# Kernel optimization log

Measured on AMD Instinct MI355X. Metric: run time of the kernel, lower is better.

The kernel has to match this reference:

```python
import jax, jax.numpy as jnp
import numpy as np

N_HEADS = 16
HEAD_DIM = 64
ROPE_THETA = 10000.0


def rotate_half(x):
    x1, x2 = jnp.split(x, 2, axis=-1)
    return jnp.concatenate([-x2, x1], axis=-1)


def setup_inputs() -> dict:
    key = jax.random.key(0)
    k0, k1, k2 = jax.random.split(key, 3)
    B, L, C = 2, 2048, 1024
    x = jax.random.normal(k0, (B, L, C), dtype=jnp.float32)
    # causal additive bias, as used by VAR-style blockwise masks (here full causal)
    causal = jnp.tril(jnp.ones((L, L), dtype=bool))
    attn_bias = jnp.where(causal, 0.0, -1e9).astype(jnp.float32)[None, None]
    position_ids = jnp.broadcast_to(jnp.arange(L, dtype=jnp.int32), (B, L))
    qkv_w = 0.02 * jax.random.normal(k1, (3 * C, C), dtype=jnp.float32)
    q_bias = jnp.zeros((C,), jnp.float32)
    v_bias = jnp.zeros((C,), jnp.float32)
    proj_w = 0.02 * jax.random.normal(k2, (C, C), dtype=jnp.float32)
    proj_b = jnp.zeros((C,), jnp.float32)
    return {"x": x, "attn_bias": attn_bias, "position_ids": position_ids,
            "qkv_w": qkv_w, "q_bias": q_bias, "v_bias": v_bias,
            "proj_w": proj_w, "proj_b": proj_b}


def reference(x, attn_bias, position_ids, qkv_w, q_bias, v_bias, proj_w, proj_b):
    B, L, C = x.shape
    H, D = N_HEADS, HEAD_DIM
    # fused QKV projection with concatenated (q_bias, 0, v_bias)
    bias = jnp.concatenate([q_bias, jnp.zeros_like(q_bias), v_bias])
    qkv = (jnp.einsum('blc,oc->blo', x, qkv_w) + bias).reshape(B, L, 3, H, D)
    q = jnp.transpose(qkv[:, :, 0], (0, 2, 1, 3))  # [B,H,L,D]
    k = jnp.transpose(qkv[:, :, 1], (0, 2, 1, 3))
    v = jnp.transpose(qkv[:, :, 2], (0, 2, 1, 3))
    # Llama rotary embedding: cos/sin [B,L,D] -> unsqueeze dim=1
    inv_freq = 1.0 / (ROPE_THETA ** (jnp.arange(0, D, 2, dtype=jnp.float32) / D))
    freqs = position_ids.astype(jnp.float32)[:, :, None] * inv_freq  # [B,L,D/2]
    emb = jnp.concatenate([freqs, freqs], axis=-1)
    cos = jnp.cos(emb)[:, None]  # [B,1,L,D]
    sin = jnp.sin(emb)[:, None]
    q = q * cos + rotate_half(q) * sin
    k = k * cos + rotate_half(k) * sin
    # slow_attn: (q*scale) @ k^T + bias -> softmax -> @ v
    scale = 0.25 / np.sqrt(D).astype(np.float32)
    attn = jnp.einsum('bhqd,bhkd->bhqk', q * scale, k) + attn_bias
    attn = jax.nn.softmax(attn, axis=-1)
    out = jnp.einsum('bhqk,bhkd->bhqd', attn, v)
    out = out.transpose(0, 2, 1, 3).reshape(B, L, C)
    return jnp.einsum('blc,oc->blo', out, proj_w) + proj_b
```

## Files before the change

### kernel.cpp

```cpp
#include <hip/hip_runtime.h>

typedef unsigned short u16;
typedef unsigned int u32;
typedef __attribute__((ext_vector_type(8))) short short8;
typedef __attribute__((ext_vector_type(4))) float f32x4;
typedef __attribute__((ext_vector_type(2))) unsigned int u32x2;
typedef __attribute__((ext_vector_type(4))) unsigned short u16x4;
typedef __attribute__((ext_vector_type(8))) unsigned short u16x8;

#define AS1 __attribute__((address_space(1)))
#define AS3 __attribute__((address_space(3)))

__device__ __forceinline__ u16 f2bf(float f) {
  u32 u = __builtin_bit_cast(u32, f);
  u32 r = u + 0x7FFFu + ((u >> 16) & 1u);
  return (u16)(r >> 16);
}
__device__ __forceinline__ float bf2f(u16 h) {
  u32 u = ((u32)h) << 16;
  return __builtin_bit_cast(float, u);
}
__device__ __forceinline__ void gload_lds16(const void* g, void* l) {
  __builtin_amdgcn_global_load_lds((AS1 void*)g, (AS3 void*)l, 16, 0, 0);
}

__device__ __forceinline__ void cvt_body(const float* __restrict__ src, u16* __restrict__ dst,
                                         int i) {
  float4 v = ((const float4*)src)[i];
  u16x4 o;
  o[0] = f2bf(v.x); o[1] = f2bf(v.y); o[2] = f2bf(v.z); o[3] = f2bf(v.w);
  ((u16x4*)dst)[i] = o;
}

__global__ __launch_bounds__(256)
void pre_kernel(const float* __restrict__ x, const float* __restrict__ w1,
                const float* __restrict__ w2, const int* __restrict__ pos,
                u16* __restrict__ x_bf, u16* __restrict__ w1_bf, u16* __restrict__ w2_bf,
                float* __restrict__ tab) {
  int bid = blockIdx.x;
  int t = threadIdx.x;
  if (bid < 4096) {
    cvt_body(x, x_bf, bid * 256 + t);
  } else if (bid < 7168) {
    cvt_body(w1, w1_bf, (bid - 4096) * 256 + t);
  } else if (bid < 8192) {
    cvt_body(w2, w2_bf, (bid - 7168) * 256 + t);
  } else {
    int idx = (bid - 8192) * 256 + t;
    int i = idx & 31;
    int bl = idx >> 5;
    float p = (float)pos[bl];
    float inv_freq = 1.0f / powf(10000.0f, (2.0f * (float)i) / 64.0f);
    float ang = p * inv_freq;
    tab[(size_t)bl * 64 + i] = cosf(ang);
    tab[(size_t)bl * 64 + 32 + i] = sinf(ang);
  }
}

template <bool OUT_BF16>
__global__ __launch_bounds__(256)
void gemm_bt_kernel(const u16* __restrict__ A, const u16* __restrict__ Bw,
                    void* __restrict__ Cout, const float* __restrict__ bias,
                    int M, int N, int K, int NXT) {
  __shared__ alignas(16) u16 As[128 * 64];
  __shared__ alignas(16) u16 Bs[128 * 64];
  const int tid = threadIdx.x;
  const int lane = tid & 63, wave = tid >> 6;
  const int wr = wave >> 1, wc = wave & 1;
  const int nblk = gridDim.x;
  const int lin = (blockIdx.x & 7) * (nblk >> 3) + (blockIdx.x >> 3);
  const int m0 = (lin / NXT) * 128, n0 = (lin % NXT) * 128;
  const int r = lane & 15, g = lane >> 4;

  f32x4 acc[4][4] = {};

  const int nk = K >> 6;
  for (int kt = 0; kt < nk; ++kt) {
    const int k0 = kt << 6;
#pragma unroll
    for (int c = 0; c < 4; ++c) {
      int i = c * 256 + tid;
      int row = i >> 3, slot = i & 7;
      int ss = slot ^ (row & 7);
      const u16* gA = A + (size_t)(m0 + row) * K + k0 + ss * 8;
      const u16* gB = Bw + (size_t)(n0 + row) * K + k0 + ss * 8;
      void* lA = (char*)As + c * 4096 + wave * 1024;
      void* lB = (char*)Bs + c * 4096 + wave * 1024;
      gload_lds16(gA, lA);
      gload_lds16(gB, lB);
    }
    __syncthreads();
#pragma unroll
    for (int kk = 0; kk < 2; ++kk) {
      short8 af[4], bf[4];
#pragma unroll
      for (int m = 0; m < 4; ++m) {
        int row = wr * 64 + m * 16 + r;
        int byte = row * 128 + (((kk * 4 + g) ^ (row & 7)) << 4);
        af[m] = *(const short8*)((const char*)As + byte);
      }
#pragma unroll
      for (int n = 0; n < 4; ++n) {
        int row = wc * 64 + n * 16 + r;
        int byte = row * 128 + (((kk * 4 + g) ^ (row & 7)) << 4);
        bf[n] = *(const short8*)((const char*)Bs + byte);
      }
#pragma unroll
      for (int m = 0; m < 4; ++m)
#pragma unroll
        for (int n = 0; n < 4; ++n)
          acc[m][n] = __builtin_amdgcn_mfma_f32_16x16x32_bf16(af[m], bf[n], acc[m][n], 0, 0, 0);
    }
    __syncthreads();
  }

  if constexpr (OUT_BF16) {
    u16* C = (u16*)Cout;
#pragma unroll
    for (int m = 0; m < 4; ++m) {
      int rg = m0 + wr * 64 + m * 16 + g * 4;
#pragma unroll
      for (int n = 0; n < 4; ++n) {
        int cg = n0 + wc * 64 + n * 16 + r;
#pragma unroll
        for (int j = 0; j < 4; ++j)
          C[(size_t)(rg + j) * N + cg] = f2bf(acc[m][n][j]);
      }
    }
  } else {
    float* C = (float*)Cout;
#pragma unroll
    for (int m = 0; m < 4; ++m) {
      int rg = m0 + wr * 64 + m * 16 + g * 4;
#pragma unroll
      for (int n = 0; n < 4; ++n) {
        int cg = n0 + wc * 64 + n * 16 + r;
        float bv = bias[cg];
#pragma unroll
        for (int j = 0; j < 4; ++j)
          C[(size_t)(rg + j) * N + cg] = acc[m][n][j] + bv;
      }
    }
  }
}

__global__ __launch_bounds__(256)
void gemm_bt64_kernel(const u16* __restrict__ A, const u16* __restrict__ Bw,
                      float* __restrict__ Cout, const float* __restrict__ bias,
                      int M, int N, int K, int NXT) {
  __shared__ alignas(16) u16 As[128 * 64];
  __shared__ alignas(16) u16 Bs[64 * 64];
  const int tid = threadIdx.x;
  const int lane = tid & 63, wave = tid >> 6;
  const int wr = wave >> 1, wc = wave & 1;
  const int nblk = gridDim.x;
  const int lin = (blockIdx.x & 7) * (nblk >> 3) + (blockIdx.x >> 3);
  const int m0 = (lin / NXT) * 128, n0 = (lin % NXT) * 64;
  const int r = lane & 15, g = lane >> 4;

  f32x4 acc[4][2] = {};

  const int nk = K >> 6;
  for (int kt = 0; kt < nk; ++kt) {
    const int k0 = kt << 6;
#pragma unroll
    for (int c = 0; c < 4; ++c) {
      int i = c * 256 + tid;
      int row = i >> 3, slot = i & 7;
      int ss = slot ^ (row & 7);
      const u16* gA = A + (size_t)(m0 + row) * K + k0 + ss * 8;
      void* lA = (char*)As + c * 4096 + wave * 1024;
      gload_lds16(gA, lA);
    }
#pragma unroll
    for (int c = 0; c < 2; ++c) {
      int i = c * 256 + tid;
      int row = i >> 3, slot = i & 7;
      int ss = slot ^ (row & 7);
      const u16* gB = Bw + (size_t)(n0 + row) * K + k0 + ss * 8;
      void* lB = (char*)Bs + c * 4096 + wave * 1024;
      gload_lds16(gB, lB);
    }
    __syncthreads();
#pragma unroll
    for (int kk = 0; kk < 2; ++kk) {
      short8 af[4], bf[2];
#pragma unroll
      for (int m = 0; m < 4; ++m) {
        int row = wr * 64 + m * 16 + r;
        int byte = row * 128 + (((kk * 4 + g) ^ (row & 7)) << 4);
        af[m] = *(const short8*)((const char*)As + byte);
      }
#pragma unroll
      for (int n = 0; n < 2; ++n) {
        int row = wc * 32 + n * 16 + r;
        int byte = row * 128 + (((kk * 4 + g) ^ (row & 7)) << 4);
        bf[n] = *(const short8*)((const char*)Bs + byte);
      }
#pragma unroll
      for (int m = 0; m < 4; ++m)
#pragma unroll
        for (int n = 0; n < 2; ++n)
          acc[m][n] = __builtin_amdgcn_mfma_f32_16x16x32_bf16(af[m], bf[n], acc[m][n], 0, 0, 0);
    }
    __syncthreads();
  }

#pragma unroll
  for (int m = 0; m < 4; ++m) {
    int rg = m0 + wr * 64 + m * 16 + g * 4;
#pragma unroll
    for (int n = 0; n < 2; ++n) {
      int cg = n0 + wc * 32 + n * 16 + r;
      float bv = bias[cg];
#pragma unroll
      for (int j = 0; j < 4; ++j)
        Cout[(size_t)(rg + j) * N + cg] = acc[m][n][j] + bv;
    }
  }
}

#define QSCALE 0.04508422002778011f
__global__ __launch_bounds__(256)
void mid_kernel(const u16* __restrict__ qkv, const float* __restrict__ tab,
                const float* __restrict__ q_bias, const float* __restrict__ v_bias,
                u16* __restrict__ Qo, u16* __restrict__ Ko, u16* __restrict__ vt) {
  __shared__ alignas(16) u16 tile[64][72];
  int bid = blockIdx.x;
  int t = threadIdx.x;
  if (bid < 4096) {
    int bl = bid;
    int b = bl >> 11, l = bl & 2047;
    const float* tr = tab + (size_t)bl * 64;
    const u16* base = qkv + (size_t)bl * 3072;
#pragma unroll
    for (int pp = 0; pp < 2; ++pp) {
      int p = t + pp * 256;
      int h = p >> 5, d = p & 31;
      float c = tr[d], s = tr[32 + d];
      size_t o = ((size_t)(b * 16 + h) * 2048 + l) * 64 + d;
      float x1 = bf2f(base[h * 64 + d]) + q_bias[h * 64 + d];
      float x2 = bf2f(base[h * 64 + d + 32]) + q_bias[h * 64 + d + 32];
      Qo[o]      = f2bf((x1 * c - x2 * s) * QSCALE);
      Qo[o + 32] = f2bf((x2 * c + x1 * s) * QSCALE);
      x1 = bf2f(base[1024 + h * 64 + d]);
      x2 = bf2f(base[1024 + h * 64 + d + 32]);
      Ko[o]      = f2bf(x1 * c - x2 * s);
      Ko[o + 32] = f2bf(x2 * c + x1 * s);
    }
  } else {
    int bid2 = bid - 4096;
    int bh = bid2 >> 5;
    int b = bh >> 4, h = bh & 15;
    int l0 = (bid2 & 31) * 64;
    int rr = t >> 2;
    int c0 = (t & 3) * 16;
    const u16* src = qkv + ((size_t)(b * 2048 + l0 + rr)) * 3072 + 2048 + h * 64 + c0;
    u16x8 a = *(const u16x8*)src;
    u16x8 bb = *(const u16x8*)(src + 8);
#pragma unroll
    for (int i = 0; i < 8; ++i) {
      a[i]  = f2bf(bf2f(a[i])  + v_bias[h * 64 + c0 + i]);
      bb[i] = f2bf(bf2f(bb[i]) + v_bias[h * 64 + c0 + 8 + i]);
    }
    *(u16x8*)&tile[rr][c0] = a;
    *(u16x8*)&tile[rr][c0 + 8] = bb;
    __syncthreads();
    int d = t >> 2;
    int lc = (t & 3) * 16;
    u16x8 o1, o2;
#pragma unroll
    for (int i = 0; i < 8; ++i) {
      o1[i] = tile[lc + i][d];
      o2[i] = tile[lc + 8 + i][d];
    }
    u16* dst = vt + ((size_t)bh * 64 + d) * 2048 + l0 + lc;
    *(u16x8*)dst = o1;
    *(u16x8*)(dst + 8) = o2;
  }
}

__global__ __launch_bounds__(256)
void attn_kernel(const u16* __restrict__ Q, const u16* __restrict__ Kmat,
                 const u16* __restrict__ Vt, u16* __restrict__ O) {
  __shared__ alignas(16) u16 Ks[2][64 * 64];
  __shared__ alignas(16) u16 Vs[2][64 * 64];
  __shared__ alignas(16) u16 Pbuf[4][1024];
  const int tid = threadIdx.x;
  const int lane = tid & 63;
  const int wave = tid >> 6;
  const int id = blockIdx.x;
  const int bh = (id & 7) + 8 * ((id >> 3) >> 4);
  const int px = (id >> 3) & 15;
  const int b = bh >> 4, h = bh & 15;
  const int r = lane & 15, g = lane >> 4;

  const u16* Kb = Kmat + (size_t)bh * 2048 * 64;
  const u16* Vb = Vt + (size_t)bh * 64 * 2048;

  const int srow0 = tid >> 3;
  const int sslot0 = (tid & 7) ^ (srow0 & 7);
  const int srow1 = srow0 + 32;
  const int sslot1 = (tid & 7) ^ (srow1 & 7);

  u16* Pw = Pbuf[wave];

  for (int seg = 0; seg < 2; ++seg) {
    const int xq = seg ? (31 - px) : px;
    const int qrow0 = xq * 64 + wave * 16;
    const int nt = xq + 1;
    const u16* Qb = Q + ((size_t)bh * 2048 + qrow0) * 64;

    short8 qf[2];
#pragma unroll
    for (int kk = 0; kk < 2; ++kk)
      qf[kk] = *(const short8*)(Qb + r * 64 + kk * 32 + g * 8);

    f32x4 o_acc[4] = {};
    float l_run = 0.f;

    gload_lds16(Kb + (size_t)srow0 * 64 + sslot0 * 8, (char*)Ks[0] + wave * 1024);
    gload_lds16(Kb + (size_t)srow1 * 64 + sslot1 * 8, (char*)Ks[0] + 4096 + wave * 1024);
    gload_lds16(Vb + (size_t)srow0 * 2048 + sslot0 * 8, (char*)Vs[0] + wave * 1024);
    gload_lds16(Vb + (size_t)srow1 * 2048 + sslot1 * 8, (char*)Vs[0] + 4096 + wave * 1024);
    __syncthreads();

    int cur = 0;
    for (int t = 0; t < nt; ++t) {
      const int kv0 = t * 64;
      if (t + 1 < nt) {
        const u16* gK = Kb + (size_t)(kv0 + 64) * 64;
        const u16* gV = Vb + (kv0 + 64);
        char* lK = (char*)Ks[cur ^ 1];
        char* lV = (char*)Vs[cur ^ 1];
        gload_lds16(gK + (size_t)srow0 * 64 + sslot0 * 8, lK + wave * 1024);
        gload_lds16(gK + (size_t)srow1 * 64 + sslot1 * 8, lK + 4096 + wave * 1024);
        gload_lds16(gV + (size_t)srow0 * 2048 + sslot0 * 8, lV + wave * 1024);
        gload_lds16(gV + (size_t)srow1 * 2048 + sslot1 * 8, lV + 4096 + wave * 1024);
      }

      f32x4 s[4] = {};
      __builtin_amdgcn_s_setprio(1);
#pragma unroll
      for (int ct = 0; ct < 4; ++ct) {
#pragma unroll
        for (int kk = 0; kk < 2; ++kk) {
          int row = ct * 16 + r;
          int byte = row * 128 + (((kk * 4 + g) ^ (row & 7)) << 4);
          short8 kf = *(const short8*)((const char*)Ks[cur] + byte);
          s[ct] = __builtin_amdgcn_mfma_f32_16x16x32_bf16(kf, qf[kk], s[ct], 0, 0, 0);
        }
      }
      __builtin_amdgcn_s_setprio(0);

      if (kv0 + 63 > qrow0) {
        int qrow = qrow0 + r;
#pragma unroll
        for (int ct = 0; ct < 4; ++ct)
#pragma unroll
          for (int j = 0; j < 4; ++j) {
            int kv = kv0 + ct * 16 + 4 * g + j;
            if (kv > qrow) s[ct][j] = -1e30f;
          }
      }

      u32x2 pk[4];
#pragma unroll
      for (int ct = 0; ct < 4; ++ct) {
        float p0 = exp2f(s[ct][0]);
        float p1 = exp2f(s[ct][1]);
        float p2 = exp2f(s[ct][2]);
        float p3 = exp2f(s[ct][3]);
        l_run += (p0 + p1) + (p2 + p3);
        u32 lo, hi;
        asm("v_cvt_pk_bf16_f32 %0, %1, %2" : "=v"(lo) : "v"(p0), "v"(p1));
        asm("v_cvt_pk_bf16_f32 %0, %1, %2" : "=v"(hi) : "v"(p2), "v"(p3));
        pk[ct][0] = lo;
        pk[ct][1] = hi;
      }

#pragma unroll
      for (int ct = 0; ct < 4; ++ct) {
        int byte = r * 128 + ((32 * ct + 8 * g) ^ ((r & 7) << 4));
        *(u32x2*)((char*)Pw + byte) = pk[ct];
      }

      __builtin_amdgcn_s_setprio(1);
#pragma unroll
      for (int kk = 0; kk < 2; ++kk) {
        int byte = r * 128 + (((kk * 4 + g) ^ (r & 7)) << 4);
        short8 pf = *(const short8*)((const char*)Pw + byte);
#pragma unroll
        for (int n = 0; n < 4; ++n) {
          int row = n * 16 + r;
          int vbyte = row * 128 + (((kk * 4 + g) ^ (row & 7)) << 4);
          short8 vf = *(const short8*)((const char*)Vs[cur] + vbyte);
          o_acc[n] = __builtin_amdgcn_mfma_f32_16x16x32_bf16(pf, vf, o_acc[n], 0, 0, 0);
        }
      }
      __builtin_amdgcn_s_setprio(0);

      __syncthreads();
      cur ^= 1;
    }

    l_run += __shfl_xor(l_run, 16, 64);
    l_run += __shfl_xor(l_run, 32, 64);
    float linv = 1.0f / l_run;
    float ij[4];
#pragma unroll
    for (int j = 0; j < 4; ++j) ij[j] = __shfl(linv, 4 * g + j, 64);
#pragma unroll
    for (int n = 0; n < 4; ++n)
#pragma unroll
      for (int j = 0; j < 4; ++j) {
        size_t idx = ((size_t)b * 2048 + qrow0 + 4 * g + j) * 1024 + h * 64 + n * 16 + r;
        O[idx] = f2bf(o_acc[n][j] * ij[j]);
      }
  }
}

extern "C" void kernel_launch(void* const* d_in, const int* in_sizes, int n_in,
                              void* d_out, int out_size, void* d_ws, size_t ws_size,
                              hipStream_t stream) {
  const float* x      = (const float*)d_in[0];
  const int*   pos    = (const int*)d_in[2];
  const float* qkv_w  = (const float*)d_in[3];
  const float* q_bias = (const float*)d_in[4];
  const float* v_bias = (const float*)d_in[5];
  const float* proj_w = (const float*)d_in[6];
  const float* proj_b = (const float*)d_in[7];
  float* out = (float*)d_out;

  char* ws = (char*)d_ws;
  u16* x_bf    = (u16*)(ws + 0);
  u16* w1_bf   = (u16*)(ws + 8388608);
  u16* w2_bf   = (u16*)(ws + 14680064);
  u16* qkv_bf  = (u16*)(ws + 16777216);
  u16* q_bf    = (u16*)(ws + 41943040);
  u16* k_bf    = (u16*)(ws + 50331648);
  u16* vt_bf   = (u16*)(ws + 58720256);
  u16* attn_bf = (u16*)(ws + 67108864);
  float* tab   = (float*)(ws + 75497472);

  pre_kernel<<<8704, 256, 0, stream>>>(x, qkv_w, proj_w, pos, x_bf, w1_bf, w2_bf, tab);
  gemm_bt_kernel<true><<<768, 256, 0, stream>>>(x_bf, w1_bf, qkv_bf, nullptr,
                                                4096, 3072, 1024, 24);
  mid_kernel<<<5120, 256, 0, stream>>>(qkv_bf, tab, q_bias, v_bias, q_bf, k_bf, vt_bf);
  attn_kernel<<<512, 256, 0, stream>>>(q_bf, k_bf, vt_bf, attn_bf);
  gemm_bt64_kernel<<<512, 256, 0, stream>>>(attn_bf, w2_bf, out, proj_b,
                                            4096, 1024, 1024, 16);
}
```

Before: 122.3 us.

## Fuse bias and RoPE into QKV GEMM epilogue and split attention blocks

The QKV GEMM epilogue now applies q/v biases, rotary embedding and the Q scale, and writes Q and K directly in head-major layout. V is written compactly and transposed by a slimmer kernel, which removes the round trip through the full bf16 qkv buffer in the old mid kernel. The RoPE table is stored as interleaved cos/sin pairs. The attention kernel no longer processes a paired short+long query tile per block; it launches one tile per block (1024 blocks), ordered longest first, for better parallelism at the cost of less even per-block work. The epilogue now does scattered 2-byte stores and per-row table loads, which may cost some GEMM efficiency.

After: 132.0 us. +8.0%, slower.

```diff
diff --git a/kernel.cpp b/kernel.cpp
--- a/kernel.cpp
+++ b/kernel.cpp
@@ -24,6 +24,8 @@
   __builtin_amdgcn_global_load_lds((AS1 void*)g, (AS3 void*)l, 16, 0, 0);
 }
 
+#define QSCALE 0.04508422002778011f
+
 __device__ __forceinline__ void cvt_body(const float* __restrict__ src, u16* __restrict__ dst,
                                          int i) {
   float4 v = ((const float4*)src)[i];
@@ -36,7 +38,7 @@
 void pre_kernel(const float* __restrict__ x, const float* __restrict__ w1,
                 const float* __restrict__ w2, const int* __restrict__ pos,
                 u16* __restrict__ x_bf, u16* __restrict__ w1_bf, u16* __restrict__ w2_bf,
-                float* __restrict__ tab) {
+                float2* __restrict__ tab2) {
   int bid = blockIdx.x;
   int t = threadIdx.x;
   if (bid < 4096) {
@@ -52,16 +54,16 @@
     float p = (float)pos[bl];
     float inv_freq = 1.0f / powf(10000.0f, (2.0f * (float)i) / 64.0f);
     float ang = p * inv_freq;
-    tab[(size_t)bl * 64 + i] = cosf(ang);
-    tab[(size_t)bl * 64 + 32 + i] = sinf(ang);
-  }
-}
-
-template <bool OUT_BF16>
+    tab2[(size_t)bl * 32 + i] = make_float2(cosf(ang), sinf(ang));
+  }
+}
+
 __global__ __launch_bounds__(256)
-void gemm_bt_kernel(const u16* __restrict__ A, const u16* __restrict__ Bw,
-                    void* __restrict__ Cout, const float* __restrict__ bias,
-                    int M, int N, int K, int NXT) {
+void gemmqkv_kernel(const u16* __restrict__ A, const u16* __restrict__ Bw,
+                    const float* __restrict__ q_bias, const float* __restrict__ v_bias,
+                    const float2* __restrict__ tab2,
+                    u16* __restrict__ Qo, u16* __restrict__ Ko, u16* __restrict__ v_comp) {
+  const int K = 1024, NXT = 24;
   __shared__ alignas(16) u16 As[128 * 64];
   __shared__ alignas(16) u16 Bs[128 * 64];
   const int tid = threadIdx.x;
@@ -74,8 +76,7 @@
 
   f32x4 acc[4][4] = {};
 
-  const int nk = K >> 6;
-  for (int kt = 0; kt < nk; ++kt) {
+  for (int kt = 0; kt < 16; ++kt) {
     const int k0 = kt << 6;
 #pragma unroll
     for (int c = 0; c < 4; ++c) {
@@ -114,31 +115,51 @@
     __syncthreads();
   }
 
-  if constexpr (OUT_BF16) {
-    u16* C = (u16*)Cout;
+  const int cgbase = n0 + wc * 64;
+  const int seg = cgbase >> 10;
+  const int h = (cgbase & 1023) >> 6;
+
+  if (seg == 2) {
 #pragma unroll
     for (int m = 0; m < 4; ++m) {
       int rg = m0 + wr * 64 + m * 16 + g * 4;
 #pragma unroll
       for (int n = 0; n < 4; ++n) {
-        int cg = n0 + wc * 64 + n * 16 + r;
+        int c10 = (cgbase & 1023) + n * 16 + r;
+        float bv = v_bias[c10];
 #pragma unroll
         for (int j = 0; j < 4; ++j)
-          C[(size_t)(rg + j) * N + cg] = f2bf(acc[m][n][j]);
+          v_comp[(size_t)(rg + j) * 1024 + c10] = f2bf(acc[m][n][j] + bv);
       }
     }
   } else {
-    float* C = (float*)Cout;
-#pragma unroll
-    for (int m = 0; m < 4; ++m) {
-      int rg = m0 + wr * 64 + m * 16 + g * 4;
-#pragma unroll
-      for (int n = 0; n < 4; ++n) {
-        int cg = n0 + wc * 64 + n * 16 + r;
-        float bv = bias[cg];
-#pragma unroll
-        for (int j = 0; j < 4; ++j)
-          C[(size_t)(rg + j) * N + cg] = acc[m][n][j] + bv;
+    u16* Out = (seg == 0) ? Qo : Ko;
+#pragma unroll
+    for (int n2 = 0; n2 < 2; ++n2) {
+      int dlo = n2 * 16 + r;
+      float b1 = (seg == 0) ? q_bias[h * 64 + dlo] : 0.f;
+      float b2 = (seg == 0) ? q_bias[h * 64 + dlo + 32] : 0.f;
+#pragma unroll
+      for (int m = 0; m < 4; ++m) {
+        int rowbase = m0 + wr * 64 + m * 16 + g * 4;
+#pragma unroll
+        for (int j = 0; j < 4; ++j) {
+          int row = rowbase + j;
+          int bb = row >> 11, l = row & 2047;
+          float2 cs = tab2[(size_t)row * 32 + dlo];
+          float x1 = acc[m][n2][j] + b1;
+          float x2 = acc[m][n2 + 2][j] + b2;
+          float y1 = x1 * cs.x - x2 * cs.y;
+          float y2 = x2 * cs.x + x1 * cs.y;
+          size_t o = ((size_t)(bb * 16 + h) * 2048 + l) * 64 + dlo;
+          if (seg == 0) {
+            Out[o]      = f2bf(y1 * QSCALE);
+            Out[o + 32] = f2bf(y2 * QSCALE);
+          } else {
+            Out[o]      = f2bf(y1);
+            Out[o + 32] = f2bf(y2);
+          }
+        }
       }
     }
   }
@@ -220,64 +241,33 @@
   }
 }
 
-#define QSCALE 0.04508422002778011f
 __global__ __launch_bounds__(256)
-void mid_kernel(const u16* __restrict__ qkv, const float* __restrict__ tab,
-                const float* __restrict__ q_bias, const float* __restrict__ v_bias,
-                u16* __restrict__ Qo, u16* __restrict__ Ko, u16* __restrict__ vt) {
+void vtr_kernel(const u16* __restrict__ v_comp, u16* __restrict__ vt) {
   __shared__ alignas(16) u16 tile[64][72];
   int bid = blockIdx.x;
+  int bh = bid >> 5;
+  int b = bh >> 4, h = bh & 15;
+  int l0 = (bid & 31) * 64;
   int t = threadIdx.x;
-  if (bid < 4096) {
-    int bl = bid;
-    int b = bl >> 11, l = bl & 2047;
-    const float* tr = tab + (size_t)bl * 64;
-    const u16* base = qkv + (size_t)bl * 3072;
-#pragma unroll
-    for (int pp = 0; pp < 2; ++pp) {
-      int p = t + pp * 256;
-      int h = p >> 5, d = p & 31;
-      float c = tr[d], s = tr[32 + d];
-      size_t o = ((size_t)(b * 16 + h) * 2048 + l) * 64 + d;
-      float x1 = bf2f(base[h * 64 + d]) + q_bias[h * 64 + d];
-      float x2 = bf2f(base[h * 64 + d + 32]) + q_bias[h * 64 + d + 32];
-      Qo[o]      = f2bf((x1 * c - x2 * s) * QSCALE);
-      Qo[o + 32] = f2bf((x2 * c + x1 * s) * QSCALE);
-      x1 = bf2f(base[1024 + h * 64 + d]);
-      x2 = bf2f(base[1024 + h * 64 + d + 32]);
-      Ko[o]      = f2bf(x1 * c - x2 * s);
-      Ko[o + 32] = f2bf(x2 * c + x1 * s);
-    }
-  } else {
-    int bid2 = bid - 4096;
-    int bh = bid2 >> 5;
-    int b = bh >> 4, h = bh & 15;
-    int l0 = (bid2 & 31) * 64;
-    int rr = t >> 2;
-    int c0 = (t & 3) * 16;
-    const u16* src = qkv + ((size_t)(b * 2048 + l0 + rr)) * 3072 + 2048 + h * 64 + c0;
-    u16x8 a = *(const u16x8*)src;
-    u16x8 bb = *(const u16x8*)(src + 8);
-#pragma unroll
-    for (int i = 0; i < 8; ++i) {
-      a[i]  = f2bf(bf2f(a[i])  + v_bias[h * 64 + c0 + i]);
-      bb[i] = f2bf(bf2f(bb[i]) + v_bias[h * 64 + c0 + 8 + i]);
-    }
-    *(u16x8*)&tile[rr][c0] = a;
-    *(u16x8*)&tile[rr][c0 + 8] = bb;
-    __syncthreads();
-    int d = t >> 2;
-    int lc = (t & 3) * 16;
-    u16x8 o1, o2;
-#pragma unroll
-    for (int i = 0; i < 8; ++i) {
-      o1[i] = tile[lc + i][d];
-      o2[i] = tile[lc + 8 + i][d];
-    }
-    u16* dst = vt + ((size_t)bh * 64 + d) * 2048 + l0 + lc;
-    *(u16x8*)dst = o1;
-    *(u16x8*)(dst + 8) = o2;
-  }
+  int rr = t >> 2;
+  int c0 = (t & 3) * 16;
+  const u16* src = v_comp + ((size_t)(b * 2048 + l0 + rr)) * 1024 + h * 64 + c0;
+  u16x8 a = *(const u16x8*)src;
+  u16x8 bb = *(const u16x8*)(src + 8);
+  *(u16x8*)&tile[rr][c0] = a;
+  *(u16x8*)&tile[rr][c0 + 8] = bb;
+  __syncthreads();
+  int d = t >> 2;
+  int lc = (t & 3) * 16;
+  u16x8 o1, o2;
+#pragma unroll
+  for (int i = 0; i < 8; ++i) {
+    o1[i] = tile[lc + i][d];
+    o2[i] = tile[lc + 8 + i][d];
+  }
+  u16* dst = vt + ((size_t)bh * 64 + d) * 2048 + l0 + lc;
+  *(u16x8*)dst = o1;
+  *(u16x8*)(dst + 8) = o2;
 }
 
 __global__ __launch_bounds__(256)
@@ -290,8 +280,9 @@
   const int lane = tid & 63;
   const int wave = tid >> 6;
   const int id = blockIdx.x;
-  const int bh = (id & 7) + 8 * ((id >> 3) >> 4);
-  const int px = (id >> 3) & 15;
+  const int xcd = id & 7, rank = id >> 3;
+  const int bh = xcd + 8 * (rank & 3);
+  const int xq = 31 - (rank >> 2);
   const int b = bh >> 4, h = bh & 15;
   const int r = lane & 15, g = lane >> 4;
 
@@ -304,120 +295,116 @@
   const int sslot1 = (tid & 7) ^ (srow1 & 7);
 
   u16* Pw = Pbuf[wave];
-
-  for (int seg = 0; seg < 2; ++seg) {
-    const int xq = seg ? (31 - px) : px;
-    const int qrow0 = xq * 64 + wave * 16;
-    const int nt = xq + 1;
-    const u16* Qb = Q + ((size_t)bh * 2048 + qrow0) * 64;
-
-    short8 qf[2];
-#pragma unroll
-    for (int kk = 0; kk < 2; ++kk)
-      qf[kk] = *(const short8*)(Qb + r * 64 + kk * 32 + g * 8);
-
-    f32x4 o_acc[4] = {};
-    float l_run = 0.f;
-
-    gload_lds16(Kb + (size_t)srow0 * 64 + sslot0 * 8, (char*)Ks[0] + wave * 1024);
-    gload_lds16(Kb + (size_t)srow1 * 64 + sslot1 * 8, (char*)Ks[0] + 4096 + wave * 1024);
-    gload_lds16(Vb + (size_t)srow0 * 2048 + sslot0 * 8, (char*)Vs[0] + wave * 1024);
-    gload_lds16(Vb + (size_t)srow1 * 2048 + sslot1 * 8, (char*)Vs[0] + 4096 + wave * 1024);
+  const int qrow0 = xq * 64 + wave * 16;
+  const int nt = xq + 1;
+  const u16* Qb = Q + ((size_t)bh * 2048 + qrow0) * 64;
+
+  short8 qf[2];
+#pragma unroll
+  for (int kk = 0; kk < 2; ++kk)
+    qf[kk] = *(const short8*)(Qb + r * 64 + kk * 32 + g * 8);
+
+  f32x4 o_acc[4] = {};
+  float l_run = 0.f;
+
+  gload_lds16(Kb + (size_t)srow0 * 64 + sslot0 * 8, (char*)Ks[0] + wave * 1024);
+  gload_lds16(Kb + (size_t)srow1 * 64 + sslot1 * 8, (char*)Ks[0] + 4096 + wave * 1024);
+  gload_lds16(Vb + (size_t)srow0 * 2048 + sslot0 * 8, (char*)Vs[0] + wave * 1024);
+  gload_lds16(Vb + (size_t)srow1 * 2048 + sslot1 * 8, (char*)Vs[0] + 4096 + wave * 1024);
+  __syncthreads();
+
+  int cur = 0;
+  for (int t = 0; t < nt; ++t) {
+    const int kv0 = t * 64;
+    if (t + 1 < nt) {
+      const u16* gK = Kb + (size_t)(kv0 + 64) * 64;
+      const u16* gV = Vb + (kv0 + 64);
+      char* lK = (char*)Ks[cur ^ 1];
+      char* lV = (char*)Vs[cur ^ 1];
+      gload_lds16(gK + (size_t)srow0 * 64 + sslot0 * 8, lK + wave * 1024);
+      gload_lds16(gK + (size_t)srow1 * 64 + sslot1 * 8, lK + 4096 + wave * 1024);
+      gload_lds16(gV + (size_t)srow0 * 2048 + sslot0 * 8, lV + wave * 1024);
+      gload_lds16(gV + (size_t)srow1 * 2048 + sslot1 * 8, lV + 4096 + wave * 1024);
+    }
+
+    f32x4 s[4] = {};
+    __builtin_amdgcn_s_setprio(1);
+#pragma unroll
+    for (int ct = 0; ct < 4; ++ct) {
+#pragma unroll
+      for (int kk = 0; kk < 2; ++kk) {
+        int row = ct * 16 + r;
+        int byte = row * 128 + (((kk * 4 + g) ^ (row & 7)) << 4);
+        short8 kf = *(const short8*)((const char*)Ks[cur] + byte);
+        s[ct] = __builtin_amdgcn_mfma_f32_16x16x32_bf16(kf, qf[kk], s[ct], 0, 0, 0);
+      }
+    }
+    __builtin_amdgcn_s_setprio(0);
+
+    if (kv0 + 63 > qrow0) {
+      int qrow = qrow0 + r;
+#pragma unroll
+      for (int ct = 0; ct < 4; ++ct)
+#pragma unroll
+        for (int j = 0; j < 4; ++j) {
+          int kv = kv0 + ct * 16 + 4 * g + j;
+          if (kv > qrow) s[ct][j] = -1e30f;
+        }
+    }
+
+    u32x2 pk[4];
+#pragma unroll
+    for (int ct = 0; ct < 4; ++ct) {
+      float p0 = exp2f(s[ct][0]);
+      float p1 = exp2f(s[ct][1]);
+      float p2 = exp2f(s[ct][2]);
+      float p3 = exp2f(s[ct][3]);
+      l_run += (p0 + p1) + (p2 + p3);
+      u32 lo, hi;
+      asm("v_cvt_pk_bf16_f32 %0, %1, %2" : "=v"(lo) : "v"(p0), "v"(p1));
+      asm("v_cvt_pk_bf16_f32 %0, %1, %2" : "=v"(hi) : "v"(p2), "v"(p3));
+      pk[ct][0] = lo;
+      pk[ct][1] = hi;
+    }
+
+#pragma unroll
+    for (int ct = 0; ct < 4; ++ct) {
+      int byte = r * 128 + ((32 * ct + 8 * g) ^ ((r & 7) << 4));
+      *(u32x2*)((char*)Pw + byte) = pk[ct];
+    }
+
+    __builtin_amdgcn_s_setprio(1);
+#pragma unroll
+    for (int kk = 0; kk < 2; ++kk) {
+      int byte = r * 128 + (((kk * 4 + g) ^ (r & 7)) << 4);
+      short8 pf = *(const short8*)((const char*)Pw + byte);
+#pragma unroll
+      for (int n = 0; n < 4; ++n) {
+        int row = n * 16 + r;
+        int vbyte = row * 128 + (((kk * 4 + g) ^ (row & 7)) << 4);
+        short8 vf = *(const short8*)((const char*)Vs[cur] + vbyte);
+        o_acc[n] = __builtin_amdgcn_mfma_f32_16x16x32_bf16(pf, vf, o_acc[n], 0, 0, 0);
+      }
+    }
+    __builtin_amdgcn_s_setprio(0);
+
     __syncthreads();
-
-    int cur = 0;
-    for (int t = 0; t < nt; ++t) {
-      const int kv0 = t * 64;
-      if (t + 1 < nt) {
-        const u16* gK = Kb + (size_t)(kv0 + 64) * 64;
-        const u16* gV = Vb + (kv0 + 64);
-        char* lK = (char*)Ks[cur ^ 1];
-        char* lV = (char*)Vs[cur ^ 1];
-        gload_lds16(gK + (size_t)srow0 * 64 + sslot0 * 8, lK + wave * 1024);
-        gload_lds16(gK + (size_t)srow1 * 64 + sslot1 * 8, lK + 4096 + wave * 1024);
-        gload_lds16(gV + (size_t)srow0 * 2048 + sslot0 * 8, lV + wave * 1024);
-        gload_lds16(gV + (size_t)srow1 * 2048 + sslot1 * 8, lV + 4096 + wave * 1024);
-      }
-
-      f32x4 s[4] = {};
-      __builtin_amdgcn_s_setprio(1);
-#pragma unroll
-      for (int ct = 0; ct < 4; ++ct) {
-#pragma unroll
-        for (int kk = 0; kk < 2; ++kk) {
-          int row = ct * 16 + r;
-          int byte = row * 128 + (((kk * 4 + g) ^ (row & 7)) << 4);
-          short8 kf = *(const short8*)((const char*)Ks[cur] + byte);
-          s[ct] = __builtin_amdgcn_mfma_f32_16x16x32_bf16(kf, qf[kk], s[ct], 0, 0, 0);
-        }
-      }
-      __builtin_amdgcn_s_setprio(0);
-
-      if (kv0 + 63 > qrow0) {
-        int qrow = qrow0 + r;
-#pragma unroll
-        for (int ct = 0; ct < 4; ++ct)
-#pragma unroll
-          for (int j = 0; j < 4; ++j) {
-            int kv = kv0 + ct * 16 + 4 * g + j;
-            if (kv > qrow) s[ct][j] = -1e30f;
-          }
-      }
-
-      u32x2 pk[4];
-#pragma unroll
-      for (int ct = 0; ct < 4; ++ct) {
-        float p0 = exp2f(s[ct][0]);
-        float p1 = exp2f(s[ct][1]);
-        float p2 = exp2f(s[ct][2]);
-        float p3 = exp2f(s[ct][3]);
-        l_run += (p0 + p1) + (p2 + p3);
-        u32 lo, hi;
-        asm("v_cvt_pk_bf16_f32 %0, %1, %2" : "=v"(lo) : "v"(p0), "v"(p1));
-        asm("v_cvt_pk_bf16_f32 %0, %1, %2" : "=v"(hi) : "v"(p2), "v"(p3));
-        pk[ct][0] = lo;
-        pk[ct][1] = hi;
-      }
-
-#pragma unroll
-      for (int ct = 0; ct < 4; ++ct) {
-        int byte = r * 128 + ((32 * ct + 8 * g) ^ ((r & 7) << 4));
-        *(u32x2*)((char*)Pw + byte) = pk[ct];
-      }
-
-      __builtin_amdgcn_s_setprio(1);
-#pragma unroll
-      for (int kk = 0; kk < 2; ++kk) {
-        int byte = r * 128 + (((kk * 4 + g) ^ (r & 7)) << 4);
-        short8 pf = *(const short8*)((const char*)Pw + byte);
-#pragma unroll
-        for (int n = 0; n < 4; ++n) {
-          int row = n * 16 + r;
-          int vbyte = row * 128 + (((kk * 4 + g) ^ (row & 7)) << 4);
-          short8 vf = *(const short8*)((const char*)Vs[cur] + vbyte);
-          o_acc[n] = __builtin_amdgcn_mfma_f32_16x16x32_bf16(pf, vf, o_acc[n], 0, 0, 0);
-        }
-      }
-      __builtin_amdgcn_s_setprio(0);
-
-      __syncthreads();
-      cur ^= 1;
-    }
-
-    l_run += __shfl_xor(l_run, 16, 64);
-    l_run += __shfl_xor(l_run, 32, 64);
-    float linv = 1.0f / l_run;
-    float ij[4];
-#pragma unroll
-    for (int j = 0; j < 4; ++j) ij[j] = __shfl(linv, 4 * g + j, 64);
-#pragma unroll
-    for (int n = 0; n < 4; ++n)
-#pragma unroll
-      for (int j = 0; j < 4; ++j) {
-        size_t idx = ((size_t)b * 2048 + qrow0 + 4 * g + j) * 1024 + h * 64 + n * 16 + r;
-        O[idx] = f2bf(o_acc[n][j] * ij[j]);
-      }
-  }
+    cur ^= 1;
+  }
+
+  l_run += __shfl_xor(l_run, 16, 64);
+  l_run += __shfl_xor(l_run, 32, 64);
+  float linv = 1.0f / l_run;
+  float ij[4];
+#pragma unroll
+  for (int j = 0; j < 4; ++j) ij[j] = __shfl(linv, 4 * g + j, 64);
+#pragma unroll
+  for (int n = 0; n < 4; ++n)
+#pragma unroll
+    for (int j = 0; j < 4; ++j) {
+      size_t idx = ((size_t)b * 2048 + qrow0 + 4 * g + j) * 1024 + h * 64 + n * 16 + r;
+      O[idx] = f2bf(o_acc[n][j] * ij[j]);
+    }
 }
 
 extern "C" void kernel_launch(void* const* d_in, const int* in_sizes, int n_in,
@@ -436,18 +423,18 @@
   u16* x_bf    = (u16*)(ws + 0);
   u16* w1_bf   = (u16*)(ws + 8388608);
   u16* w2_bf   = (u16*)(ws + 14680064);
-  u16* qkv_bf  = (u16*)(ws + 16777216);
-  u16* q_bf    = (u16*)(ws + 41943040);
-  u16* k_bf    = (u16*)(ws + 50331648);
-  u16* vt_bf   = (u16*)(ws + 58720256);
-  u16* attn_bf = (u16*)(ws + 67108864);
-  float* tab   = (float*)(ws + 75497472);
-
-  pre_kernel<<<8704, 256, 0, stream>>>(x, qkv_w, proj_w, pos, x_bf, w1_bf, w2_bf, tab);
-  gemm_bt_kernel<true><<<768, 256, 0, stream>>>(x_bf, w1_bf, qkv_bf, nullptr,
-                                                4096, 3072, 1024, 24);
-  mid_kernel<<<5120, 256, 0, stream>>>(qkv_bf, tab, q_bias, v_bias, q_bf, k_bf, vt_bf);
-  attn_kernel<<<512, 256, 0, stream>>>(q_bf, k_bf, vt_bf, attn_bf);
+  u16* v_comp  = (u16*)(ws + 16777216);
+  u16* q_bf    = (u16*)(ws + 25165824);
+  u16* k_bf    = (u16*)(ws + 33554432);
+  u16* vt_bf   = (u16*)(ws + 41943040);
+  u16* attn_bf = (u16*)(ws + 50331648);
+  float2* tab2 = (float2*)(ws + 58720256);
+
+  pre_kernel<<<8704, 256, 0, stream>>>(x, qkv_w, proj_w, pos, x_bf, w1_bf, w2_bf, tab2);
+  gemmqkv_kernel<<<768, 256, 0, stream>>>(x_bf, w1_bf, q_bias, v_bias, tab2,
+                                          q_bf, k_bf, v_comp);
+  vtr_kernel<<<1024, 256, 0, stream>>>(v_comp, vt_bf);
+  attn_kernel<<<1024, 256, 0, stream>>>(q_bf, k_bf, vt_bf, attn_bf);
   gemm_bt64_kernel<<<512, 256, 0, stream>>>(attn_bf, w2_bf, out, proj_b,
                                             4096, 1024, 1024, 16);
 }
```
